# Kernel optimization log

Hardware: AMD Instinct MI355X
Metric: run time of the kernel (lower is better)

Reference implementation:

```python
import jax, jax.numpy as jnp
import numpy as np

D_MODEL = 1024
D_STATE = 16
K = 4           # conv kernel size
EXPAND = 2
D_INNER = EXPAND * D_MODEL
DT_RANK = 64    # ceil(D_MODEL / 16)
EPS = 1e-5
BATCH, L = 2, 1024


def setup_inputs() -> dict:
    key = jax.random.key(0)
    ks = jax.random.split(key, 11)
    s = 0.02
    return {
        "hidden_states": jax.random.normal(ks[0], (BATCH, L, D_MODEL), jnp.float32),
        "norm_w": jnp.ones((D_MODEL,), jnp.float32),
        "W_in": jax.random.normal(ks[1], (D_MODEL, 2 * D_INNER), jnp.float32) * s,
        "conv_w": jax.random.normal(ks[2], (D_INNER, K), jnp.float32) * 0.1,
        "conv_b": jax.random.normal(ks[3], (D_INNER,), jnp.float32) * s,
        "W_x": jax.random.normal(ks[4], (D_INNER, DT_RANK + 2 * D_STATE), jnp.float32) * s,
        "W_dt": jax.random.normal(ks[5], (DT_RANK, D_INNER), jnp.float32) * s,
        "b_dt": jax.random.normal(ks[6], (D_INNER,), jnp.float32) * s,
        # A kept negative for scan stability (init choice; math identical)
        "A": -jnp.exp(jax.random.normal(ks[7], (D_INNER, D_STATE), jnp.float32) * 0.5),
        "D": jax.random.normal(ks[8], (D_INNER,), jnp.float32) * s,
        "W_out": jax.random.normal(ks[9], (D_INNER, D_MODEL), jnp.float32) * s,
    }


def reference(hidden_states, norm_w, W_in, conv_w, conv_b, W_x, W_dt, b_dt, A, D, W_out):
    x0 = hidden_states                                # [B, L, d_model]
    # RMSNorm
    h = x0 * jax.lax.rsqrt(jnp.mean(x0 * x0, axis=-1, keepdims=True) + EPS) * norm_w
    # in_proj -> (x, res)
    x, res = jnp.split(h @ W_in, 2, axis=-1)          # each [B, L, d_inner]
    Bsz, Lq, _ = x.shape
    # causal depthwise conv1d (padding K-1 on left, truncate to L)
    xp = jnp.pad(x, ((0, 0), (K - 1, 0), (0, 0)))
    xc = sum(xp[:, j:j + Lq, :] * conv_w[:, j] for j in range(K)) + conv_b
    x = jax.nn.silu(xc)
    # x_proj -> delta, B, C
    xdbl = x @ W_x
    dlt, Bm, Cm = jnp.split(xdbl, [DT_RANK, DT_RANK + D_STATE], axis=-1)
    delta = jax.nn.softplus(dlt @ W_dt + b_dt)        # [B, L, d_inner]
    # selective scan
    deltaA = jnp.exp(jnp.einsum('bld,dn->bldn', delta, A))        # [B,L,d_in,n]
    dbu = (delta * x)[..., None] * Bm[:, :, None, :]              # [B,L,d_in,n]

    def step(carry, inp):
        dA, db, c = inp
        carry = dA * carry + db                       # [B, d_in, n]
        y = jnp.einsum('bdn,bn->bd', carry, c)
        return carry, y

    init = jnp.zeros((Bsz, D_INNER, D_STATE), x.dtype)
    _, ys = jax.lax.scan(step, init,
                         (deltaA.transpose(1, 0, 2, 3),
                          dbu.transpose(1, 0, 2, 3),
                          Cm.transpose(1, 0, 2)))
    y = ys.transpose(1, 0, 2) + x * D                 # [B, L, d_inner]
    y = y * jax.nn.silu(res)
    return x0 + y @ W_out
```

## Files before the change

### kernel.cpp

```cpp
#include <hip/hip_runtime.h>
#include <hip/hip_bf16.h>
#include <math.h>

#define BATCH 2
#define LSEQ 1024
#define DMODEL 1024
#define DINNER 2048
#define DSTATE 16
#define DTRANK 64
#define NROWS (BATCH * LSEQ)
#define XROW 128
#define NC 32
#define TCH (LSEQ / NC)

typedef __bf16 bf16;
typedef __attribute__((ext_vector_type(8))) __bf16 bf16x8;
typedef __attribute__((ext_vector_type(4))) float floatx4;

#define TM 128
#define TN 128
#define TK 32

__device__ __forceinline__ void glds16(const bf16* g, bf16* l) {
    __builtin_amdgcn_global_load_lds(
        (const __attribute__((address_space(1))) void*)g,
        (__attribute__((address_space(3))) void*)l, 16, 0, 0);
}

template<int MODE, bool BF16OUT>
__global__ __launch_bounds__(256) void gemm_bf16_kernel(
    const bf16* __restrict__ A, int lda,
    const bf16* __restrict__ Bt, int ldb,
    void* __restrict__ Cv, int ldc,
    int Ksplit,
    const float* __restrict__ bias,
    const float* __restrict__ resid, int ldr)
{
    __shared__ __attribute__((aligned(16))) bf16 As[TM * TK];
    __shared__ __attribute__((aligned(16))) bf16 Bs[TN * TK];

    const int tid  = threadIdx.x;
    const int lane = tid & 63;
    const int wave = tid >> 6;
    const int l15  = lane & 15;
    const int quad = lane >> 4;
    const int wm   = (wave >> 1) * 64;
    const int wn   = (wave & 1) * 64;

    const int row0 = blockIdx.y * TM;
    const int col0 = blockIdx.x * TN;
    const long kbase = (long)blockIdx.z * Ksplit;

    const int c0   = wave * 64 + lane;
    const int crow = c0 >> 2;
    const int ckq  = (c0 & 3) * 8;

    const bf16* gA0 = A  + (size_t)(row0 + crow) * lda + kbase + ckq;
    const bf16* gA1 = gA0 + (size_t)64 * lda;
    const bf16* gB0 = Bt + (size_t)(col0 + crow) * ldb + kbase + ckq;
    const bf16* gB1 = gB0 + (size_t)64 * ldb;

    bf16* lA0 = As + wave * 64 * 8;
    bf16* lA1 = As + (256 + wave * 64) * 8;
    bf16* lB0 = Bs + wave * 64 * 8;
    bf16* lB1 = Bs + (256 + wave * 64) * 8;

    floatx4 acc[4][4];
    #pragma unroll
    for (int i = 0; i < 4; ++i)
        #pragma unroll
        for (int j = 0; j < 4; ++j)
            acc[i][j] = (floatx4){0.f, 0.f, 0.f, 0.f};

    const int kiters = Ksplit / TK;
    for (int kk = 0; kk < kiters; ++kk) {
        __syncthreads();
        glds16(gA0, lA0);
        glds16(gA1, lA1);
        glds16(gB0, lB0);
        glds16(gB1, lB1);
        gA0 += TK; gA1 += TK; gB0 += TK; gB1 += TK;
        __syncthreads();

        bf16x8 af[4], bfr[4];
        #pragma unroll
        for (int i = 0; i < 4; ++i)
            af[i] = *(const bf16x8*)&As[(wm + i * 16 + l15) * TK + quad * 8];
        #pragma unroll
        for (int j = 0; j < 4; ++j)
            bfr[j] = *(const bf16x8*)&Bs[(wn + j * 16 + l15) * TK + quad * 8];
        #pragma unroll
        for (int i = 0; i < 4; ++i)
            #pragma unroll
            for (int j = 0; j < 4; ++j)
                acc[i][j] = __builtin_amdgcn_mfma_f32_16x16x32_bf16(
                                af[i], bfr[j], acc[i][j], 0, 0, 0);
    }

    #pragma unroll
    for (int i = 0; i < 4; ++i) {
        #pragma unroll
        for (int j = 0; j < 4; ++j) {
            const int gn = col0 + wn + j * 16 + l15;
            #pragma unroll
            for (int r = 0; r < 4; ++r) {
                const int gm = row0 + wm + i * 16 + quad * 4 + r;
                float v = acc[i][j][r];
                if (MODE == 1) {
                    v += bias[gn];
                    v = (v > 20.0f) ? v : log1pf(__expf(v));
                }
                if (MODE == 2) v += resid[(size_t)gm * ldr + gn];
                if (MODE == 3) {
                    atomicAdd(&((float*)Cv)[(size_t)gm * ldc + gn], v);
                } else if (BF16OUT) {
                    ((bf16*)Cv)[(size_t)gm * ldc + gn] = (bf16)v;
                } else {
                    ((float*)Cv)[(size_t)gm * ldc + gn] = v;
                }
            }
        }
    }
}

__global__ __launch_bounds__(256) void transpose_bf16_kernel(
    const float* __restrict__ W, bf16* __restrict__ Wt,
    int K, int N, int Npad)
{
    __shared__ float tile[32][33];
    const int n0 = blockIdx.x * 32;
    const int k0 = blockIdx.y * 32;
    const int tx = threadIdx.x & 31;
    const int ty = threadIdx.x >> 5;
    #pragma unroll
    for (int i = 0; i < 32; i += 8) {
        int k = k0 + ty + i, n = n0 + tx;
        tile[ty + i][tx] = (k < K && n < N) ? W[(size_t)k * N + n] : 0.0f;
    }
    __syncthreads();
    #pragma unroll
    for (int i = 0; i < 32; i += 8) {
        int n = n0 + ty + i, k = k0 + tx;
        if (n < Npad && k < K)
            Wt[(size_t)n * K + k] = (bf16)tile[tx][ty + i];
    }
}

__global__ __launch_bounds__(256) void rmsnorm_kernel(
    const float* __restrict__ x, const float* __restrict__ w,
    bf16* __restrict__ h)
{
    int row = blockIdx.x;
    int tid = threadIdx.x;
    const float* xr = x + (size_t)row * DMODEL;
    float4 v = *(const float4*)(xr + tid * 4);
    float ss = v.x * v.x + v.y * v.y + v.z * v.z + v.w * v.w;
    #pragma unroll
    for (int m = 32; m >= 1; m >>= 1) ss += __shfl_xor(ss, m);
    __shared__ float ws[4];
    if ((tid & 63) == 0) ws[tid >> 6] = ss;
    __syncthreads();
    float total = ws[0] + ws[1] + ws[2] + ws[3];
    float scale = rsqrtf(total * (1.0f / DMODEL) + 1e-5f);
    float4 wv = *(const float4*)(w + tid * 4);
    union { bf16 b[4]; uint2 u; } pk;
    pk.b[0] = (bf16)(v.x * scale * wv.x);
    pk.b[1] = (bf16)(v.y * scale * wv.y);
    pk.b[2] = (bf16)(v.z * scale * wv.z);
    pk.b[3] = (bf16)(v.w * scale * wv.w);
    *(uint2*)(h + (size_t)row * DMODEL + tid * 4) = pk.u;
}

__global__ __launch_bounds__(256) void conv_silu_kernel(
    const bf16* __restrict__ xz, const float* __restrict__ conv_w,
    const float* __restrict__ conv_b, bf16* __restrict__ xc)
{
    int idx = blockIdx.x * 256 + threadIdx.x;
    int c = idx & (DINNER - 1);
    int row = idx >> 11;
    int l = row & (LSEQ - 1);
    float w0 = conv_w[c * 4 + 0];
    float w1 = conv_w[c * 4 + 1];
    float w2 = conv_w[c * 4 + 2];
    float w3 = conv_w[c * 4 + 3];
    const bf16* xr = xz + (size_t)row * (2 * DINNER) + c;
    float acc = conv_b[c] + (float)xr[0] * w3;
    if (l >= 1) acc += (float)xr[-1 * 2 * DINNER] * w2;
    if (l >= 2) acc += (float)xr[-2 * 2 * DINNER] * w1;
    if (l >= 3) acc += (float)xr[-3 * 2 * DINNER] * w0;
    float s = acc / (1.0f + __expf(-acc));
    xc[idx] = (bf16)s;
}

__global__ __launch_bounds__(256) void dtconv_kernel(
    const float* __restrict__ xdbl, bf16* __restrict__ dt)
{
    int idx = blockIdx.x * 256 + threadIdx.x;
    int row = idx >> 6, j = idx & 63;
    dt[idx] = (bf16)xdbl[(size_t)row * XROW + j];
}

template<bool FINAL>
__global__ __launch_bounds__(256) void scan_chunk_kernel(
    const float* __restrict__ delta,
    const bf16* __restrict__ xc,
    const float* __restrict__ xdbl,
    const float* __restrict__ A,
    float* __restrict__ Pbuf,
    float* __restrict__ Sbuf,
    const bf16* __restrict__ xz,
    const float* __restrict__ Dp,
    bf16* __restrict__ ybf)
{
    __shared__ float sBC[TCH][32];
    const int tid   = threadIdx.x;
    const int chunk = blockIdx.x;
    const int d     = blockIdx.y * 256 + tid;
    const int b     = blockIdx.z;
    const int row0  = b * LSEQ + chunk * TCH;

    {
        int t = tid >> 3, c4 = (tid & 7) * 4;
        *(float4*)&sBC[t][c4] =
            *(const float4*)&xdbl[(size_t)(row0 + t) * XROW + DTRANK + c4];
    }

    float Ad[16];
    #pragma unroll
    for (int j = 0; j < 4; ++j) {
        float4 av = *(const float4*)&A[(size_t)d * DSTATE + j * 4];
        Ad[j*4+0] = av.x; Ad[j*4+1] = av.y; Ad[j*4+2] = av.z; Ad[j*4+3] = av.w;
    }

    const size_t psoff = ((size_t)(b * NC + chunk) * DINNER + d) * DSTATE;
    float S[16], P[16];
    if (FINAL) {
        #pragma unroll
        for (int j = 0; j < 4; ++j) {
            float4 sv = *(const float4*)&Sbuf[psoff + j * 4];
            S[j*4+0] = sv.x; S[j*4+1] = sv.y; S[j*4+2] = sv.z; S[j*4+3] = sv.w;
        }
    } else {
        #pragma unroll
        for (int n = 0; n < 16; ++n) { S[n] = 0.0f; P[n] = 1.0f; }
    }
    float Dpd = FINAL ? Dp[d] : 0.0f;

    __syncthreads();

    #pragma unroll 2
    for (int t = 0; t < TCH; ++t) {
        const size_t row = (size_t)(row0 + t);
        float dv = delta[row * DINNER + d];
        float xv = (float)xc[row * DINNER + d];
        float u  = dv * xv;
        float yp[4] = {0.f, 0.f, 0.f, 0.f};
        #pragma unroll
        for (int n = 0; n < 16; ++n) {
            float dA = __expf(dv * Ad[n]);
            S[n] = dA * S[n] + u * sBC[t][n];
            if (FINAL) {
                yp[n & 3] += S[n] * sBC[t][16 + n];
            } else {
                P[n] *= dA;
            }
        }
        if (FINAL) {
            float y = (yp[0] + yp[1]) + (yp[2] + yp[3]);
            float res = (float)xz[row * (2 * DINNER) + DINNER + d];
            float sres = res / (1.0f + __expf(-res));
            ybf[row * DINNER + d] = (bf16)((y + xv * Dpd) * sres);
        }
    }

    if (!FINAL) {
        #pragma unroll
        for (int j = 0; j < 4; ++j) {
            *(float4*)&Pbuf[psoff + j * 4] =
                (float4){P[j*4+0], P[j*4+1], P[j*4+2], P[j*4+3]};
            *(float4*)&Sbuf[psoff + j * 4] =
                (float4){S[j*4+0], S[j*4+1], S[j*4+2], S[j*4+3]};
        }
    }
}

__global__ __launch_bounds__(256) void scan_combine_kernel(
    const float* __restrict__ Pbuf, float* __restrict__ Sbuf)
{
    int gid = blockIdx.x * 256 + threadIdx.x;
    int b = gid >> 15;
    int dn = gid & 32767;
    float carry = 0.0f;
    for (int k = 0; k < NC; ++k) {
        size_t off = ((size_t)(b * NC + k) << 15) + dn;
        float pk = Pbuf[off];
        float sk = Sbuf[off];
        Sbuf[off] = carry;
        carry = pk * carry + sk;
    }
}

extern "C" void kernel_launch(void* const* d_in, const int* in_sizes, int n_in,
                              void* d_out, int out_size, void* d_ws, size_t ws_size,
                              hipStream_t stream)
{
    const float* x0     = (const float*)d_in[0];
    const float* norm_w = (const float*)d_in[1];
    const float* W_in   = (const float*)d_in[2];
    const float* conv_w = (const float*)d_in[3];
    const float* conv_b = (const float*)d_in[4];
    const float* W_x    = (const float*)d_in[5];
    const float* W_dt   = (const float*)d_in[6];
    const float* b_dt   = (const float*)d_in[7];
    const float* A      = (const float*)d_in[8];
    const float* Dp     = (const float*)d_in[9];
    const float* W_out  = (const float*)d_in[10];
    float* out = (float*)d_out;

    char* p = (char*)d_ws;
    bf16*  xz_bf = (bf16*)p;            p += (size_t)NROWS * 2 * DINNER * 2;
    float* xdbl  = (float*)p;           p += (size_t)NROWS * XROW * 4;
    float* delta = (float*)p;           p += (size_t)NROWS * DINNER * 4;
    float* Pbuf  = (float*)p;           p += (size_t)BATCH * NC * DINNER * 16 * 4;
    float* Sbuf  = (float*)p;           p += (size_t)BATCH * NC * DINNER * 16 * 4;
    bf16*  h_bf  = (bf16*)p;            p += (size_t)NROWS * DMODEL * 2;
    bf16*  xc_bf = (bf16*)p;            p += (size_t)NROWS * DINNER * 2;
    bf16*  y_bf  = (bf16*)p;            p += (size_t)NROWS * DINNER * 2;
    bf16*  WinT  = (bf16*)p;            p += (size_t)(2*DINNER) * DMODEL * 2;
    bf16*  WxT   = (bf16*)p;            p += (size_t)XROW * DINNER * 2;
    bf16*  WdtT  = (bf16*)p;            p += (size_t)DINNER * DTRANK * 2;
    bf16*  WoutT = (bf16*)p;            p += (size_t)DMODEL * DINNER * 2;
    bf16*  dt_bf = (bf16*)p;            p += (size_t)NROWS * DTRANK * 2;

    transpose_bf16_kernel<<<dim3(128, 32), 256, 0, stream>>>(W_in,  WinT,  DMODEL, 2*DINNER, 2*DINNER);
    transpose_bf16_kernel<<<dim3(4, 64),   256, 0, stream>>>(W_x,   WxT,   DINNER, 96, XROW);
    transpose_bf16_kernel<<<dim3(64, 2),   256, 0, stream>>>(W_dt,  WdtT,  DTRANK, DINNER, DINNER);
    transpose_bf16_kernel<<<dim3(32, 64),  256, 0, stream>>>(W_out, WoutT, DINNER, DMODEL, DMODEL);

    rmsnorm_kernel<<<NROWS, 256, 0, stream>>>(x0, norm_w, h_bf);

    gemm_bf16_kernel<0, true><<<dim3(32, 16, 1), 256, 0, stream>>>(
        h_bf, DMODEL, WinT, DMODEL, xz_bf, 2*DINNER, DMODEL, nullptr, nullptr, 0);

    conv_silu_kernel<<<(NROWS * DINNER) / 256, 256, 0, stream>>>(xz_bf, conv_w, conv_b, xc_bf);

    hipMemsetAsync(xdbl, 0, (size_t)NROWS * XROW * 4, stream);
    gemm_bf16_kernel<3, false><<<dim3(1, 16, 8), 256, 0, stream>>>(
        xc_bf, DINNER, WxT, DINNER, xdbl, XROW, DINNER / 8, nullptr, nullptr, 0);

    dtconv_kernel<<<(NROWS * DTRANK) / 256, 256, 0, stream>>>(xdbl, dt_bf);

    gemm_bf16_kernel<1, false><<<dim3(16, 16, 1), 256, 0, stream>>>(
        dt_bf, DTRANK, WdtT, DTRANK, delta, DINNER, DTRANK, b_dt, nullptr, 0);

    dim3 sgrid(NC, DINNER / 256, BATCH);
    scan_chunk_kernel<false><<<sgrid, 256, 0, stream>>>(
        delta, xc_bf, xdbl, A, Pbuf, Sbuf, nullptr, nullptr, nullptr);
    scan_combine_kernel<<<(BATCH * DINNER * DSTATE) / 256, 256, 0, stream>>>(Pbuf, Sbuf);
    scan_chunk_kernel<true><<<sgrid, 256, 0, stream>>>(
        delta, xc_bf, xdbl, A, Pbuf, Sbuf, xz_bf, Dp, y_bf);

    gemm_bf16_kernel<2, false><<<dim3(8, 16, 1), 256, 0, stream>>>(
        y_bf, DINNER, WoutT, DINNER, out, DMODEL, DINNER, nullptr, x0, DMODEL);
}
```

Baseline: 306.2 us.

## Template GEMM on tile sizes, swizzle LDS, replace atomic split-K with reduce kernel

The GEMM kernel is now templated on N-tile width and K-step (BK=64). LDS chunk placement uses an XOR swizzle to reduce bank conflicts. The x_proj split-K drops the memset and atomicAdd path: each K-split writes its partial tile to a separate buffer, and a new reduce kernel sums the partials, emitting dt in bf16 and B/C in a compact fp32 layout for the scan. The out-projection switches to 64-wide N tiles so twice as many blocks run. This adds workspace and an 8-way partial read in exchange for removing atomics and improving occupancy.

```diff
diff --git a/kernel.cpp b/kernel.cpp
--- a/kernel.cpp
+++ b/kernel.cpp
@@ -17,17 +17,7 @@
 typedef __attribute__((ext_vector_type(8))) __bf16 bf16x8;
 typedef __attribute__((ext_vector_type(4))) float floatx4;
 
-#define TM 128
-#define TN 128
-#define TK 32
-
-__device__ __forceinline__ void glds16(const bf16* g, bf16* l) {
-    __builtin_amdgcn_global_load_lds(
-        (const __attribute__((address_space(1))) void*)g,
-        (__attribute__((address_space(3))) void*)l, 16, 0, 0);
-}
-
-template<int MODE, bool BF16OUT>
+template<int MODE, bool BF16OUT, int TN_, int BK_>
 __global__ __launch_bounds__(256) void gemm_bf16_kernel(
     const bf16* __restrict__ A, int lda,
     const bf16* __restrict__ Bt, int ldb,
@@ -36,8 +26,15 @@
     const float* __restrict__ bias,
     const float* __restrict__ resid, int ldr)
 {
-    __shared__ __attribute__((aligned(16))) bf16 As[TM * TK];
-    __shared__ __attribute__((aligned(16))) bf16 Bs[TN * TK];
+    constexpr int TMc  = 128;
+    constexpr int CA   = BK_ / 8;
+    constexpr int ISSA = TMc * BK_ * 2 / 4096;
+    constexpr int ISSB = TN_ * BK_ * 2 / 4096;
+    constexpr int NB   = TN_ / 32;
+    constexpr int NH   = BK_ / 32;
+
+    __shared__ __attribute__((aligned(16))) bf16 As[TMc * BK_];
+    __shared__ __attribute__((aligned(16))) bf16 Bs[TN_ * BK_];
 
     const int tid  = threadIdx.x;
     const int lane = tid & 63;
@@ -45,62 +42,85 @@
     const int l15  = lane & 15;
     const int quad = lane >> 4;
     const int wm   = (wave >> 1) * 64;
-    const int wn   = (wave & 1) * 64;
-
-    const int row0 = blockIdx.y * TM;
-    const int col0 = blockIdx.x * TN;
+    const int wn   = (wave & 1) * (TN_ / 2);
+
+    const int row0 = blockIdx.y * TMc;
+    const int col0 = blockIdx.x * TN_;
     const long kbase = (long)blockIdx.z * Ksplit;
 
-    const int c0   = wave * 64 + lane;
-    const int crow = c0 >> 2;
-    const int ckq  = (c0 & 3) * 8;
-
-    const bf16* gA0 = A  + (size_t)(row0 + crow) * lda + kbase + ckq;
-    const bf16* gA1 = gA0 + (size_t)64 * lda;
-    const bf16* gB0 = Bt + (size_t)(col0 + crow) * ldb + kbase + ckq;
-    const bf16* gB1 = gB0 + (size_t)64 * ldb;
-
-    bf16* lA0 = As + wave * 64 * 8;
-    bf16* lA1 = As + (256 + wave * 64) * 8;
-    bf16* lB0 = Bs + wave * 64 * 8;
-    bf16* lB1 = Bs + (256 + wave * 64) * 8;
-
-    floatx4 acc[4][4];
+    const bf16* gA[ISSA]; bf16* lA[ISSA];
+    const bf16* gB[ISSB]; bf16* lB[ISSB];
+    #pragma unroll
+    for (int i = 0; i < ISSA; ++i) {
+        int c = i * 256 + wave * 64 + lane;
+        int r = c / CA;
+        int kc = (c % CA) ^ (r % CA);
+        gA[i] = A + (size_t)(row0 + r) * lda + kbase + kc * 8;
+        lA[i] = As + (size_t)(i * 256 + wave * 64) * 8;
+    }
+    #pragma unroll
+    for (int i = 0; i < ISSB; ++i) {
+        int c = i * 256 + wave * 64 + lane;
+        int r = c / CA;
+        int kc = (c % CA) ^ (r % CA);
+        gB[i] = Bt + (size_t)(col0 + r) * ldb + kbase + kc * 8;
+        lB[i] = Bs + (size_t)(i * 256 + wave * 64) * 8;
+    }
+
+    floatx4 acc[4][NB];
     #pragma unroll
     for (int i = 0; i < 4; ++i)
         #pragma unroll
-        for (int j = 0; j < 4; ++j)
+        for (int j = 0; j < NB; ++j)
             acc[i][j] = (floatx4){0.f, 0.f, 0.f, 0.f};
 
-    const int kiters = Ksplit / TK;
+    const int kiters = Ksplit / BK_;
     for (int kk = 0; kk < kiters; ++kk) {
         __syncthreads();
-        glds16(gA0, lA0);
-        glds16(gA1, lA1);
-        glds16(gB0, lB0);
-        glds16(gB1, lB1);
-        gA0 += TK; gA1 += TK; gB0 += TK; gB1 += TK;
+        #pragma unroll
+        for (int i = 0; i < ISSA; ++i) {
+            __builtin_amdgcn_global_load_lds(
+                (const __attribute__((address_space(1))) void*)gA[i],
+                (__attribute__((address_space(3))) void*)lA[i], 16, 0, 0);
+            gA[i] += BK_;
+        }
+        #pragma unroll
+        for (int i = 0; i < ISSB; ++i) {
+            __builtin_amdgcn_global_load_lds(
+                (const __attribute__((address_space(1))) void*)gB[i],
+                (__attribute__((address_space(3))) void*)lB[i], 16, 0, 0);
+            gB[i] += BK_;
+        }
         __syncthreads();
 
-        bf16x8 af[4], bfr[4];
-        #pragma unroll
-        for (int i = 0; i < 4; ++i)
-            af[i] = *(const bf16x8*)&As[(wm + i * 16 + l15) * TK + quad * 8];
-        #pragma unroll
-        for (int j = 0; j < 4; ++j)
-            bfr[j] = *(const bf16x8*)&Bs[(wn + j * 16 + l15) * TK + quad * 8];
-        #pragma unroll
-        for (int i = 0; i < 4; ++i)
+        #pragma unroll
+        for (int h = 0; h < NH; ++h) {
+            bf16x8 af[4], bfr[NB];
             #pragma unroll
-            for (int j = 0; j < 4; ++j)
-                acc[i][j] = __builtin_amdgcn_mfma_f32_16x16x32_bf16(
-                                af[i], bfr[j], acc[i][j], 0, 0, 0);
+            for (int i = 0; i < 4; ++i) {
+                int r = wm + i * 16 + l15;
+                af[i] = *(const bf16x8*)&As[(size_t)r * BK_ +
+                          (((h * 4 + quad) ^ (r % CA)) * 8)];
+            }
+            #pragma unroll
+            for (int j = 0; j < NB; ++j) {
+                int r = wn + j * 16 + l15;
+                bfr[j] = *(const bf16x8*)&Bs[(size_t)r * BK_ +
+                           (((h * 4 + quad) ^ (r % CA)) * 8)];
+            }
+            #pragma unroll
+            for (int i = 0; i < 4; ++i)
+                #pragma unroll
+                for (int j = 0; j < NB; ++j)
+                    acc[i][j] = __builtin_amdgcn_mfma_f32_16x16x32_bf16(
+                                    af[i], bfr[j], acc[i][j], 0, 0, 0);
+        }
     }
 
     #pragma unroll
     for (int i = 0; i < 4; ++i) {
         #pragma unroll
-        for (int j = 0; j < 4; ++j) {
+        for (int j = 0; j < NB; ++j) {
             const int gn = col0 + wn + j * 16 + l15;
             #pragma unroll
             for (int r = 0; r < 4; ++r) {
@@ -111,8 +131,8 @@
                     v = (v > 20.0f) ? v : log1pf(__expf(v));
                 }
                 if (MODE == 2) v += resid[(size_t)gm * ldr + gn];
-                if (MODE == 3) {
-                    atomicAdd(&((float*)Cv)[(size_t)gm * ldc + gn], v);
+                if (MODE == 4) {
+                    ((float*)Cv)[(size_t)blockIdx.z * ldr + (size_t)gm * ldc + gn] = v;
                 } else if (BF16OUT) {
                     ((bf16*)Cv)[(size_t)gm * ldc + gn] = (bf16)v;
                 } else {
@@ -192,19 +212,25 @@
     xc[idx] = (bf16)s;
 }
 
-__global__ __launch_bounds__(256) void dtconv_kernel(
-    const float* __restrict__ xdbl, bf16* __restrict__ dt)
+__global__ __launch_bounds__(256) void xproj_reduce_kernel(
+    const float* __restrict__ Pw, bf16* __restrict__ dt,
+    float* __restrict__ BC)
 {
     int idx = blockIdx.x * 256 + threadIdx.x;
-    int row = idx >> 6, j = idx & 63;
-    dt[idx] = (bf16)xdbl[(size_t)row * XROW + j];
+    int row = idx >> 7, c = idx & 127;
+    float s = 0.0f;
+    #pragma unroll
+    for (int k = 0; k < 8; ++k)
+        s += Pw[(size_t)k * NROWS * XROW + idx];
+    if (c < 64) dt[(size_t)row * 64 + c] = (bf16)s;
+    else if (c < 96) BC[(size_t)row * 32 + (c - 64)] = s;
 }
 
 template<bool FINAL>
 __global__ __launch_bounds__(256) void scan_chunk_kernel(
     const float* __restrict__ delta,
     const bf16* __restrict__ xc,
-    const float* __restrict__ xdbl,
+    const float* __restrict__ BC,
     const float* __restrict__ A,
     float* __restrict__ Pbuf,
     float* __restrict__ Sbuf,
@@ -221,8 +247,7 @@
 
     {
         int t = tid >> 3, c4 = (tid & 7) * 4;
-        *(float4*)&sBC[t][c4] =
-            *(const float4*)&xdbl[(size_t)(row0 + t) * XROW + DTRANK + c4];
+        *(float4*)&sBC[t][c4] = *(const float4*)&BC[(size_t)(row0 + t) * 32 + c4];
     }
 
     float Ad[16];
@@ -319,7 +344,8 @@
 
     char* p = (char*)d_ws;
     bf16*  xz_bf = (bf16*)p;            p += (size_t)NROWS * 2 * DINNER * 2;
-    float* xdbl  = (float*)p;           p += (size_t)NROWS * XROW * 4;
+    float* Pw    = (float*)p;           p += (size_t)8 * NROWS * XROW * 4;
+    float* BC    = (float*)p;           p += (size_t)NROWS * 32 * 4;
     float* delta = (float*)p;           p += (size_t)NROWS * DINNER * 4;
     float* Pbuf  = (float*)p;           p += (size_t)BATCH * NC * DINNER * 16 * 4;
     float* Sbuf  = (float*)p;           p += (size_t)BATCH * NC * DINNER * 16 * 4;
@@ -339,27 +365,26 @@
 
     rmsnorm_kernel<<<NROWS, 256, 0, stream>>>(x0, norm_w, h_bf);
 
-    gemm_bf16_kernel<0, true><<<dim3(32, 16, 1), 256, 0, stream>>>(
+    gemm_bf16_kernel<0, true, 128, 64><<<dim3(32, 16, 1), 256, 0, stream>>>(
         h_bf, DMODEL, WinT, DMODEL, xz_bf, 2*DINNER, DMODEL, nullptr, nullptr, 0);
 
     conv_silu_kernel<<<(NROWS * DINNER) / 256, 256, 0, stream>>>(xz_bf, conv_w, conv_b, xc_bf);
 
-    hipMemsetAsync(xdbl, 0, (size_t)NROWS * XROW * 4, stream);
-    gemm_bf16_kernel<3, false><<<dim3(1, 16, 8), 256, 0, stream>>>(
-        xc_bf, DINNER, WxT, DINNER, xdbl, XROW, DINNER / 8, nullptr, nullptr, 0);
-
-    dtconv_kernel<<<(NROWS * DTRANK) / 256, 256, 0, stream>>>(xdbl, dt_bf);
-
-    gemm_bf16_kernel<1, false><<<dim3(16, 16, 1), 256, 0, stream>>>(
+    gemm_bf16_kernel<4, false, 128, 64><<<dim3(1, 16, 8), 256, 0, stream>>>(
+        xc_bf, DINNER, WxT, DINNER, Pw, XROW, DINNER / 8, nullptr, nullptr, NROWS * XROW);
+
+    xproj_reduce_kernel<<<(NROWS * XROW) / 256, 256, 0, stream>>>(Pw, dt_bf, BC);
+
+    gemm_bf16_kernel<1, false, 128, 64><<<dim3(16, 16, 1), 256, 0, stream>>>(
         dt_bf, DTRANK, WdtT, DTRANK, delta, DINNER, DTRANK, b_dt, nullptr, 0);
 
     dim3 sgrid(NC, DINNER / 256, BATCH);
     scan_chunk_kernel<false><<<sgrid, 256, 0, stream>>>(
-        delta, xc_bf, xdbl, A, Pbuf, Sbuf, nullptr, nullptr, nullptr);
+        delta, xc_bf, BC, A, Pbuf, Sbuf, nullptr, nullptr, nullptr);
     scan_combine_kernel<<<(BATCH * DINNER * DSTATE) / 256, 256, 0, stream>>>(Pbuf, Sbuf);
     scan_chunk_kernel<true><<<sgrid, 256, 0, stream>>>(
-        delta, xc_bf, xdbl, A, Pbuf, Sbuf, xz_bf, Dp, y_bf);
-
-    gemm_bf16_kernel<2, false><<<dim3(8, 16, 1), 256, 0, stream>>>(
+        delta, xc_bf, BC, A, Pbuf, Sbuf, xz_bf, Dp, y_bf);
+
+    gemm_bf16_kernel<2, false, 64, 64><<<dim3(16, 16, 1), 256, 0, stream>>>(
         y_bf, DINNER, WoutT, DINNER, out, DMODEL, DINNER, nullptr, x0, DMODEL);
 }
```

Result: faster. 278.5 us (-9.1%).
